# Optimization experiments

Hardware: AMD Instinct MI355X
Metric: run time of the kernel (lower is better)

The kernel has to match this reference:

```python
import jax, jax.numpy as jnp
import numpy as np

B, D, C = 4096, 4096, 1024


def setup_inputs() -> dict:
    key = jax.random.key(0)
    kx, kw = jax.random.split(key)
    x = jax.random.normal(kx, (B, D), dtype=jnp.float32)
    # kaiming_normal_ with nonlinearity='relu': std = sqrt(2 / fan_in)
    W = jax.random.normal(kw, (C, D), dtype=jnp.float32) * jnp.sqrt(2.0 / D)
    return {"x": x, "W": W}


def reference(x, W):
    # Original: -( (x[:, :, None] - W.T[None, :, :])**2 ).mean(axis=1)
    d = x.shape[1]
    x_sq = jnp.sum(x * x, axis=1, keepdims=True)        # [B, 1]
    w_sq = jnp.sum(W * W, axis=1)[None, :]              # [1, C]
    cross = jnp.einsum('bd,cd->bc', x, W)               # [B, C] tensor-core GEMM
    return -(x_sq - 2.0 * cross + w_sq) / d
```

## Files before the change

kernel.cpp:

```cpp
#include <hip/hip_runtime.h>
#include <hip/hip_bf16.h>


typedef float f32x4 __attribute__((ext_vector_type(4)));
typedef float f32x2 __attribute__((ext_vector_type(2)));
typedef float f32x16 __attribute__((ext_vector_type(16)));
typedef int i32x4 __attribute__((ext_vector_type(4)));
typedef int i32x8 __attribute__((ext_vector_type(8)));

#define BDIM 4096
#define DDIM 4096
#define CDIM 1024
#define TM 128
#define TN 128
#define BK 64
#define KSPLIT 4
#define NIT ((DDIM / KSPLIT) / BK)
#define SCALE 32.0f
#define INV_SS (1.0f/1024.0f)
#define PSCALE 0.0625f

#define SYNC_LGKM() asm volatile("s_waitcnt lgkmcnt(0)\n\ts_barrier" ::: "memory")

__global__ __launch_bounds__(256) void cvt_rowsq(
    const float* __restrict__ x, const float* __restrict__ W,
    unsigned char* __restrict__ xb, unsigned char* __restrict__ wb,
    float* __restrict__ xsq, float* __restrict__ wsq)
{
    const int lane = threadIdx.x & 63;
    const int row = blockIdx.x * 4 + (threadIdx.x >> 6);

    const float* src;
    unsigned char* dst;
    float* sq;
    if (row < BDIM) {
        src = x + (size_t)row * DDIM;
        dst = xb + (size_t)row * DDIM;
        sq = xsq + row;
    } else {
        int r = row - BDIM;
        src = W + (size_t)r * DDIM;
        dst = wb + (size_t)r * DDIM;
        sq = wsq + r;
    }

    const float4* s4 = (const float4*)src;
    unsigned int* d4 = (unsigned int*)dst;
    float a = 0.f;
    #pragma unroll
    for (int s = 0; s < DDIM / 4 / 64; ++s) {
        float4 f = s4[lane + 64 * s];
        a += f.x * f.x + f.y * f.y + f.z * f.z + f.w * f.w;
        unsigned int p = 0;
        p = __builtin_amdgcn_cvt_pk_fp8_f32(f.x * SCALE, f.y * SCALE, p, false);
        p = __builtin_amdgcn_cvt_pk_fp8_f32(f.z * SCALE, f.w * SCALE, p, true);
        d4[lane + 64 * s] = p;
    }
    #pragma unroll
    for (int off = 32; off > 0; off >>= 1) a += __shfl_down(a, off);
    if (lane == 0) *sq = a;
}

struct PrefA { i32x4 a0, a1; };
struct PrefB { i32x4 b00, b01, b10, b11; };

__device__ __forceinline__ i32x8 cat8(i32x4 lo, i32x4 hi) {
    return __builtin_shufflevector(lo, hi, 0, 1, 2, 3, 4, 5, 6, 7);
}

#define MXMFMA(A, Bv, C)                                                  \
    __builtin_amdgcn_mfma_scale_f32_32x32x64_f8f6f4(                      \
        (A), (Bv), (C), 0, 0, 0, 0x7F7F7F7F, 0, 0x7F7F7F7F)

__global__ __launch_bounds__(256, 3) void gemm_eucl(
    const unsigned char* __restrict__ xb,
    const unsigned char* __restrict__ wb,
    unsigned int* __restrict__ part)
{
    __shared__ unsigned char sm[2 * 8192];

    const int tid = threadIdx.x;
    const int lane = tid & 63;
    const int wid = tid >> 6;
    const int bm = blockIdx.x * TM;
    const int bn = blockIdx.y * TN;
    const int ks = blockIdx.z * (DDIM / KSPLIT);
    const int wm = (wid >> 1) * 64;
    const int wn = (wid & 1) * 64;

    const int r0 = tid >> 2, c = tid & 3;
    const unsigned int oA0 = (unsigned int)((bm + r0) * DDIM + ks + c * 16);
    const unsigned int oA1 = oA0 + 64u * DDIM;

    const int wo0 = r0 * 64 + ((c ^ ((r0 >> 1) & 3)) * 16);

    const int sswz = (lane >> 1) & 3;
    const int c0 = (lane >> 5) * 2;
    const int m0 = wm + (lane & 31);
    const int aof0 = m0 * 64 + ((c0 ^ sswz) * 16);
    const int aof1 = m0 * 64 + (((c0 + 1) ^ sswz) * 16);

    const unsigned char* pB0 =
        wb + (size_t)(bn + wn + (lane & 31)) * DDIM + ks + (lane >> 5) * 32;
    const unsigned char* pB1 = pB0 + (size_t)32 * DDIM;

    f32x16 acc[4] = {};

#define ALOAD(S, KT)                                                     \
    do {                                                                 \
        (S).a0 = *(const i32x4*)(xb + oA0 + (KT) * BK);                  \
        (S).a1 = *(const i32x4*)(xb + oA1 + (KT) * BK);                  \
    } while (0)

#define BLOAD(T, KT)                                                     \
    do {                                                                 \
        (T).b00 = *(const i32x4*)(pB0 + (KT) * BK);                      \
        (T).b01 = *(const i32x4*)(pB0 + (KT) * BK + 16);                 \
        (T).b10 = *(const i32x4*)(pB1 + (KT) * BK);                      \
        (T).b11 = *(const i32x4*)(pB1 + (KT) * BK + 16);                 \
    } while (0)

#define AWRITE(buf, S)                                                   \
    do {                                                                 \
        unsigned char* sA = sm + (buf) * 8192;                           \
        *(i32x4*)(sA + wo0) = (S).a0;                                    \
        *(i32x4*)(sA + wo0 + 4096) = (S).a1;                             \
    } while (0)

#define COMPUTE(buf, T)                                                  \
    do {                                                                 \
        const unsigned char* sA = sm + (buf) * 8192;                     \
        i32x8 fb0 = cat8((T).b00, (T).b01);                              \
        i32x8 fb1 = cat8((T).b10, (T).b11);                              \
        i32x8 fa0 = cat8(*(const i32x4*)(sA + aof0),                     \
                         *(const i32x4*)(sA + aof1));                    \
        acc[0] = MXMFMA(fa0, fb0, acc[0]);                               \
        i32x8 fa1 = cat8(*(const i32x4*)(sA + aof0 + 2048),              \
                         *(const i32x4*)(sA + aof1 + 2048));             \
        acc[1] = MXMFMA(fa0, fb1, acc[1]);                               \
        acc[2] = MXMFMA(fa1, fb0, acc[2]);                               \
        acc[3] = MXMFMA(fa1, fb1, acc[3]);                               \
    } while (0)

    PrefA SA[3];
    PrefB SB[3];
    ALOAD(SA[0], 0); BLOAD(SB[0], 0);
    ALOAD(SA[1], 1); BLOAD(SB[1], 1);
    ALOAD(SA[2], 2);
    AWRITE(0, SA[0]);
    SYNC_LGKM();

    #pragma unroll
    for (int k = 0; k < NIT - 1; ++k) {
        if (k < NIT - 3) ALOAD(SA[k % 3], k + 3);
        if (k < NIT - 2) BLOAD(SB[(k + 2) % 3], k + 2);
        COMPUTE(k & 1, SB[k % 3]);
        AWRITE((k + 1) & 1, SA[(k + 1) % 3]);
        SYNC_LGKM();
    }
    COMPUTE((NIT - 1) & 1, SB[(NIT - 1) % 3]);

    unsigned int* p = part
        + (((size_t)blockIdx.z * 256 + (blockIdx.x * 8 + blockIdx.y)) * 16) * 256;
    #pragma unroll
    for (int t = 0; t < 4; ++t)
        #pragma unroll
        for (int g = 0; g < 4; ++g) {
            unsigned int pk = 0;
            pk = __builtin_amdgcn_cvt_pk_fp8_f32(
                acc[t][g * 4 + 0] * PSCALE, acc[t][g * 4 + 1] * PSCALE, pk, false);
            pk = __builtin_amdgcn_cvt_pk_fp8_f32(
                acc[t][g * 4 + 2] * PSCALE, acc[t][g * 4 + 3] * PSCALE, pk, true);
            p[(t * 4 + g) * 256 + tid] = pk;
        }
#undef ALOAD
#undef BLOAD
#undef AWRITE
#undef COMPUTE
}

__global__ __launch_bounds__(256) void reduce_out(
    const unsigned int* __restrict__ part, const float* __restrict__ xsq,
    const float* __restrict__ wsq, float* __restrict__ out)
{
    const int bid = blockIdx.x;
    const int bb = bid >> 1;
    const int f0 = (bid & 1) * 8;
    const int t = threadIdx.x;
    const int lane = t & 63;
    const int wid = t >> 6;
    const int bm = (bb >> 3) * TM, bn = (bb & 7) * TN;
    const int wm = (wid >> 1) * 64, wn = (wid & 1) * 64;
    const size_t sl = (size_t)256 * 16 * 256;
    const float c1 = 2.0f * 16.0f * INV_SS / (float)DDIM;
    const float c2 = 1.0f / (float)DDIM;

    #pragma unroll
    for (int f = f0; f < f0 + 8; ++f) {
        size_t o = ((size_t)bb * 16 + f) * 256 + t;
        f32x2 s01 = {0.f, 0.f}, s23 = {0.f, 0.f};
        #pragma unroll
        for (int z = 0; z < KSPLIT; ++z) {
            unsigned int u = part[o + (size_t)z * sl];
            s01 += __builtin_amdgcn_cvt_pk_f32_fp8(u, false);
            s23 += __builtin_amdgcn_cvt_pk_f32_fp8(u, true);
        }
        int t4 = f >> 2, g = f & 3;
        int it = t4 >> 1, jt = t4 & 1;
        int gn = bn + wn + jt * 32 + (lane & 31);
        float wv = wsq[gn];
        int gm0 = bm + wm + it * 32 + (lane >> 5) * 4 + g * 8;
        float sv[4] = {s01.x, s01.y, s23.x, s23.y};
        #pragma unroll
        for (int r = 0; r < 4; ++r) {
            out[(size_t)(gm0 + r) * CDIM + gn] = sv[r] * c1 - (xsq[gm0 + r] + wv) * c2;
        }
    }
}

__global__ void fallback_kernel(const float* __restrict__ x, const float* __restrict__ W,
                                float* __restrict__ out)
{
    int c = blockIdx.x * blockDim.x + threadIdx.x;
    int b = blockIdx.y;
    if (c >= CDIM) return;
    const float* xr = x + (size_t)b * DDIM;
    const float* wr = W + (size_t)c * DDIM;
    float xs = 0.f, ws = 0.f, cr = 0.f;
    for (int d = 0; d < DDIM; ++d) {
        float xv = xr[d], wv = wr[d];
        xs += xv * xv; ws += wv * wv; cr += xv * wv;
    }
    out[(size_t)b * CDIM + c] = (2.0f * cr - xs - ws) / (float)DDIM;
}

extern "C" void kernel_launch(void* const* d_in, const int* in_sizes, int n_in,
                              void* d_out, int out_size, void* d_ws, size_t ws_size,
                              hipStream_t stream) {
    const float* x = (const float*)d_in[0];
    const float* W = (const float*)d_in[1];
    float* out = (float*)d_out;

    size_t need = (size_t)(BDIM + CDIM) * DDIM
                + (size_t)(BDIM + CDIM) * sizeof(float)
                + (size_t)KSPLIT * BDIM * CDIM;
    if (ws_size < need) {
        fallback_kernel<<<dim3(CDIM / 256, BDIM), 256, 0, stream>>>(x, W, out);
        return;
    }

    unsigned char* xb = (unsigned char*)d_ws;
    unsigned char* wb = xb + (size_t)BDIM * DDIM;
    float* xsq = (float*)(wb + (size_t)CDIM * DDIM);
    float* wsq = xsq + BDIM;
    unsigned int* part = (unsigned int*)(wsq + CDIM);

    cvt_rowsq<<<(BDIM + CDIM) / 4, 256, 0, stream>>>(x, W, xb, wb, xsq, wsq);
    gemm_eucl<<<dim3(BDIM / TM, CDIM / TN, KSPLIT), 256, 0, stream>>>(xb, wb, part);
    reduce_out<<<512, 256, 0, stream>>>(part, xsq, wsq, out);
}
```

Measured before the change: 159.8 us.

## Enlarge GEMM tiles to 256x256 with direct global-to-LDS loads for A and B

Grows the FP8 GEMM block tile from 128x128 to 256x256 with 512 threads (8 waves, each computing 128x64). Both A and B are now staged into double-buffered LDS via global_load_lds instead of register prefetch, with vmcnt-based waits and s_setprio around the MFMA cluster. The partial-sum layout and reduce kernel indexing are updated to match. This aims to raise operand reuse and cut per-thread register staging. In exchange there are fewer blocks (256 instead of 1024), which may underfill the CUs, and LDS use is larger.

```diff
diff --git a/kernel.cpp b/kernel.cpp
--- a/kernel.cpp
+++ b/kernel.cpp
@@ -11,8 +11,8 @@
 #define BDIM 4096
 #define DDIM 4096
 #define CDIM 1024
-#define TM 128
-#define TN 128
+#define TM 256
+#define TN 256
 #define BK 64
 #define KSPLIT 4
 #define NIT ((DDIM / KSPLIT) / BK)
@@ -20,7 +20,7 @@
 #define INV_SS (1.0f/1024.0f)
 #define PSCALE 0.0625f
 
-#define SYNC_LGKM() asm volatile("s_waitcnt lgkmcnt(0)\n\ts_barrier" ::: "memory")
+#define WAITV(N) asm volatile("s_waitcnt vmcnt(" #N ")" ::: "memory")
 
 __global__ __launch_bounds__(256) void cvt_rowsq(
     const float* __restrict__ x, const float* __restrict__ W,
@@ -61,8 +61,6 @@
     if (lane == 0) *sq = a;
 }
 
-struct PrefA { i32x4 a0, a1; };
-struct PrefB { i32x4 b00, b01, b10, b11; };
 
 __device__ __forceinline__ i32x8 cat8(i32x4 lo, i32x4 hi) {
     return __builtin_shufflevector(lo, hi, 0, 1, 2, 3, 4, 5, 6, 7);
@@ -72,111 +70,113 @@
     __builtin_amdgcn_mfma_scale_f32_32x32x64_f8f6f4(                      \
         (A), (Bv), (C), 0, 0, 0, 0x7F7F7F7F, 0, 0x7F7F7F7F)
 
-__global__ __launch_bounds__(256, 3) void gemm_eucl(
+#define GLOAD16(gp, lp)                                                   \
+    __builtin_amdgcn_global_load_lds(                                     \
+        (const __attribute__((address_space(1))) void*)(gp),              \
+        (__attribute__((address_space(3))) void*)(lp), 16, 0, 0)
+
+__global__ __launch_bounds__(512, 2) void gemm_eucl(
     const unsigned char* __restrict__ xb,
     const unsigned char* __restrict__ wb,
     unsigned int* __restrict__ part)
 {
-    __shared__ unsigned char sm[2 * 8192];
+    __shared__ unsigned char sm[2 * 32768];
 
     const int tid = threadIdx.x;
     const int lane = tid & 63;
-    const int wid = tid >> 6;
+    const int w = tid >> 6;
+    const int wr = w >> 2;
+    const int wc = w & 3;
     const int bm = blockIdx.x * TM;
     const int bn = blockIdx.y * TN;
     const int ks = blockIdx.z * (DDIM / KSPLIT);
-    const int wm = (wid >> 1) * 64;
-    const int wn = (wid & 1) * 64;
-
-    const int r0 = tid >> 2, c = tid & 3;
-    const unsigned int oA0 = (unsigned int)((bm + r0) * DDIM + ks + c * 16);
-    const unsigned int oA1 = oA0 + 64u * DDIM;
-
-    const int wo0 = r0 * 64 + ((c ^ ((r0 >> 1) & 3)) * 16);
-
-    const int sswz = (lane >> 1) & 3;
-    const int c0 = (lane >> 5) * 2;
-    const int m0 = wm + (lane & 31);
-    const int aof0 = m0 * 64 + ((c0 ^ sswz) * 16);
-    const int aof1 = m0 * 64 + (((c0 + 1) ^ sswz) * 16);
-
-    const unsigned char* pB0 =
-        wb + (size_t)(bn + wn + (lane & 31)) * DDIM + ks + (lane >> 5) * 32;
-    const unsigned char* pB1 = pB0 + (size_t)32 * DDIM;
-
-    f32x16 acc[4] = {};
-
-#define ALOAD(S, KT)                                                     \
-    do {                                                                 \
-        (S).a0 = *(const i32x4*)(xb + oA0 + (KT) * BK);                  \
-        (S).a1 = *(const i32x4*)(xb + oA1 + (KT) * BK);                  \
+
+    const int srow = w * 32 + (lane >> 2);
+    const int schunk = ((lane & 3) ^ ((lane >> 3) & 3)) * 16;
+    const unsigned char* gA0 = xb + (size_t)(bm + srow) * DDIM + ks + schunk;
+    const unsigned char* gA1 = gA0 + (size_t)16 * DDIM;
+    const unsigned char* gB0 = wb + (size_t)(bn + srow) * DDIM + ks + schunk;
+    const unsigned char* gB1 = gB0 + (size_t)16 * DDIM;
+    unsigned char* lA0 = sm + w * 2048;
+    unsigned char* lA1 = lA0 + 1024;
+    unsigned char* lB0 = sm + 16384 + w * 2048;
+    unsigned char* lB1 = lB0 + 1024;
+
+#define STAGE_A(buf, t)                                                   \
+    do {                                                                  \
+        GLOAD16(gA0 + (t) * BK, lA0 + (buf) * 32768);                     \
+        GLOAD16(gA1 + (t) * BK, lA1 + (buf) * 32768);                     \
     } while (0)
-
-#define BLOAD(T, KT)                                                     \
-    do {                                                                 \
-        (T).b00 = *(const i32x4*)(pB0 + (KT) * BK);                      \
-        (T).b01 = *(const i32x4*)(pB0 + (KT) * BK + 16);                 \
-        (T).b10 = *(const i32x4*)(pB1 + (KT) * BK);                      \
-        (T).b11 = *(const i32x4*)(pB1 + (KT) * BK + 16);                 \
+#define STAGE_B(buf, t)                                                   \
+    do {                                                                  \
+        GLOAD16(gB0 + (t) * BK, lB0 + (buf) * 32768);                     \
+        GLOAD16(gB1 + (t) * BK, lB1 + (buf) * 32768);                     \
     } while (0)
 
-#define AWRITE(buf, S)                                                   \
-    do {                                                                 \
-        unsigned char* sA = sm + (buf) * 8192;                           \
-        *(i32x4*)(sA + wo0) = (S).a0;                                    \
-        *(i32x4*)(sA + wo0 + 4096) = (S).a1;                             \
-    } while (0)
-
-#define COMPUTE(buf, T)                                                  \
-    do {                                                                 \
-        const unsigned char* sA = sm + (buf) * 8192;                     \
-        i32x8 fb0 = cat8((T).b00, (T).b01);                              \
-        i32x8 fb1 = cat8((T).b10, (T).b11);                              \
-        i32x8 fa0 = cat8(*(const i32x4*)(sA + aof0),                     \
-                         *(const i32x4*)(sA + aof1));                    \
-        acc[0] = MXMFMA(fa0, fb0, acc[0]);                               \
-        i32x8 fa1 = cat8(*(const i32x4*)(sA + aof0 + 2048),              \
-                         *(const i32x4*)(sA + aof1 + 2048));             \
-        acc[1] = MXMFMA(fa0, fb1, acc[1]);                               \
-        acc[2] = MXMFMA(fa1, fb0, acc[2]);                               \
-        acc[3] = MXMFMA(fa1, fb1, acc[3]);                               \
-    } while (0)
-
-    PrefA SA[3];
-    PrefB SB[3];
-    ALOAD(SA[0], 0); BLOAD(SB[0], 0);
-    ALOAD(SA[1], 1); BLOAD(SB[1], 1);
-    ALOAD(SA[2], 2);
-    AWRITE(0, SA[0]);
-    SYNC_LGKM();
-
-    #pragma unroll
-    for (int k = 0; k < NIT - 1; ++k) {
-        if (k < NIT - 3) ALOAD(SA[k % 3], k + 3);
-        if (k < NIT - 2) BLOAD(SB[(k + 2) % 3], k + 2);
-        COMPUTE(k & 1, SB[k % 3]);
-        AWRITE((k + 1) & 1, SA[(k + 1) % 3]);
-        SYNC_LGKM();
-    }
-    COMPUTE((NIT - 1) & 1, SB[(NIT - 1) % 3]);
-
-    unsigned int* p = part
-        + (((size_t)blockIdx.z * 256 + (blockIdx.x * 8 + blockIdx.y)) * 16) * 256;
-    #pragma unroll
-    for (int t = 0; t < 4; ++t)
+    const int s_rd = ((lane & 31) >> 1) & 3;
+    const int c0s = ((lane >> 5) * 2) ^ s_rd;
+    const unsigned char* aR0 = sm + (wr * 128 + (lane & 31)) * 64 + c0s * 16;
+    const unsigned char* aR1 = sm + (wr * 128 + (lane & 31)) * 64 + (c0s ^ 1) * 16;
+    const unsigned char* bR0 = sm + 16384 + (wc * 64 + (lane & 31)) * 64 + c0s * 16;
+    const unsigned char* bR1 = sm + 16384 + (wc * 64 + (lane & 31)) * 64 + (c0s ^ 1) * 16;
+
+    f32x16 acc[8] = {};
+
+    STAGE_B(0, 0);
+    STAGE_A(0, 0);
+    WAITV(0);
+    __builtin_amdgcn_s_barrier();
+
+    i32x8 fb0, fb1;
+
+    #pragma unroll
+    for (int t = 0; t < NIT; ++t) {
+        const int p = t & 1;
+        const int po = p * 32768;
+        if (t + 1 < NIT) STAGE_B(p ^ 1, t + 1);
+        fb0 = cat8(*(const i32x4*)(bR0 + po), *(const i32x4*)(bR1 + po));
+        fb1 = cat8(*(const i32x4*)(bR0 + po + 2048), *(const i32x4*)(bR1 + po + 2048));
+        if (t + 1 < NIT) WAITV(2);
+        else             WAITV(0);
+        __builtin_amdgcn_s_barrier();
+        if (t + 1 < NIT) STAGE_A(p ^ 1, t + 1);
+        {
+            i32x8 fa0 = cat8(*(const i32x4*)(aR0 + po), *(const i32x4*)(aR1 + po));
+            i32x8 fa1 = cat8(*(const i32x4*)(aR0 + po + 2048), *(const i32x4*)(aR1 + po + 2048));
+            i32x8 fa2 = cat8(*(const i32x4*)(aR0 + po + 4096), *(const i32x4*)(aR1 + po + 4096));
+            i32x8 fa3 = cat8(*(const i32x4*)(aR0 + po + 6144), *(const i32x4*)(aR1 + po + 6144));
+            __builtin_amdgcn_s_setprio(1);
+            acc[0] = MXMFMA(fa0, fb0, acc[0]);
+            acc[1] = MXMFMA(fa0, fb1, acc[1]);
+            acc[2] = MXMFMA(fa1, fb0, acc[2]);
+            acc[3] = MXMFMA(fa1, fb1, acc[3]);
+            acc[4] = MXMFMA(fa2, fb0, acc[4]);
+            acc[5] = MXMFMA(fa2, fb1, acc[5]);
+            acc[6] = MXMFMA(fa3, fb0, acc[6]);
+            acc[7] = MXMFMA(fa3, fb1, acc[7]);
+            __builtin_amdgcn_s_setprio(0);
+        }
+        if (t + 1 < NIT) {
+            WAITV(2);
+            __builtin_amdgcn_s_barrier();
+        }
+    }
+
+    const int bb = blockIdx.x * 4 + blockIdx.y;
+    unsigned int* p = part + ((size_t)blockIdx.z * 64 + bb) * (32 * 512);
+    #pragma unroll
+    for (int f = 0; f < 8; ++f)
         #pragma unroll
         for (int g = 0; g < 4; ++g) {
             unsigned int pk = 0;
             pk = __builtin_amdgcn_cvt_pk_fp8_f32(
-                acc[t][g * 4 + 0] * PSCALE, acc[t][g * 4 + 1] * PSCALE, pk, false);
+                acc[f][g * 4 + 0] * PSCALE, acc[f][g * 4 + 1] * PSCALE, pk, false);
             pk = __builtin_amdgcn_cvt_pk_fp8_f32(
-                acc[t][g * 4 + 2] * PSCALE, acc[t][g * 4 + 3] * PSCALE, pk, true);
-            p[(t * 4 + g) * 256 + tid] = pk;
-        }
-#undef ALOAD
-#undef BLOAD
-#undef AWRITE
-#undef COMPUTE
+                acc[f][g * 4 + 2] * PSCALE, acc[f][g * 4 + 3] * PSCALE, pk, true);
+            p[(f * 4 + g) * 512 + tid] = pk;
+        }
+#undef STAGE_A
+#undef STAGE_B
 }
 
 __global__ __launch_bounds__(256) void reduce_out(
@@ -184,20 +184,20 @@
     const float* __restrict__ wsq, float* __restrict__ out)
 {
     const int bid = blockIdx.x;
-    const int bb = bid >> 1;
-    const int f0 = (bid & 1) * 8;
+    const int bb = bid >> 3;
+    const int w = bid & 7;
+    const int wr = w >> 2, wc = w & 3;
     const int t = threadIdx.x;
     const int lane = t & 63;
-    const int wid = t >> 6;
-    const int bm = (bb >> 3) * TM, bn = (bb & 7) * TN;
-    const int wm = (wid >> 1) * 64, wn = (wid & 1) * 64;
-    const size_t sl = (size_t)256 * 16 * 256;
+    const int g = t >> 6;
+    const int bm = (bb >> 2) * TM, bn = (bb & 3) * TN;
+    const size_t sl = (size_t)64 * 32 * 512;
     const float c1 = 2.0f * 16.0f * INV_SS / (float)DDIM;
     const float c2 = 1.0f / (float)DDIM;
 
     #pragma unroll
-    for (int f = f0; f < f0 + 8; ++f) {
-        size_t o = ((size_t)bb * 16 + f) * 256 + t;
+    for (int f = 0; f < 8; ++f) {
+        size_t o = ((size_t)bb * 32 + f * 4 + g) * 512 + w * 64 + lane;
         f32x2 s01 = {0.f, 0.f}, s23 = {0.f, 0.f};
         #pragma unroll
         for (int z = 0; z < KSPLIT; ++z) {
@@ -205,11 +205,10 @@
             s01 += __builtin_amdgcn_cvt_pk_f32_fp8(u, false);
             s23 += __builtin_amdgcn_cvt_pk_f32_fp8(u, true);
         }
-        int t4 = f >> 2, g = f & 3;
-        int it = t4 >> 1, jt = t4 & 1;
-        int gn = bn + wn + jt * 32 + (lane & 31);
+        int i = f >> 1, j = f & 1;
+        int gn = bn + wc * 64 + j * 32 + (lane & 31);
         float wv = wsq[gn];
-        int gm0 = bm + wm + it * 32 + (lane >> 5) * 4 + g * 8;
+        int gm0 = bm + wr * 128 + i * 32 + 8 * g + 4 * (lane >> 5);
         float sv[4] = {s01.x, s01.y, s23.x, s23.y};
         #pragma unroll
         for (int r = 0; r < 4; ++r) {
@@ -256,6 +255,6 @@
     unsigned int* part = (unsigned int*)(wsq + CDIM);
 
     cvt_rowsq<<<(BDIM + CDIM) / 4, 256, 0, stream>>>(x, W, xb, wb, xsq, wsq);
-    gemm_eucl<<<dim3(BDIM / TM, CDIM / TN, KSPLIT), 256, 0, stream>>>(xb, wb, part);
+    gemm_eucl<<<dim3(BDIM / TM, CDIM / TN, KSPLIT), 512, 0, stream>>>(xb, wb, part);
     reduce_out<<<512, 256, 0, stream>>>(part, xsq, wsq, out);
 }
```

New measurement: 135.4 us. 1.18x faster.
